# Kernel tuning notes

Measured on AMD Instinct MI355X. Metric: run time of the kernel, lower is better.

## Reference

```python
import jax, jax.numpy as jnp
import numpy as np


def setup_inputs() -> dict:
    key = jax.random.key(0)
    x = jax.random.normal(key, (8, 16, 256, 256, 3, 3), dtype=jnp.float32)
    return {"x": x, "padding_dim": 1}


def reference(x, padding_dim):
    """Vectorized SPD identity-pad: borders get eye(3), interior copies x.

    x: [B, C, H, W, 3, 3] -> [B, C, H+2p, W+2p, 3, 3]
    Faithful to the original quadruple-nested-loop `padding` function.
    """
    p = padding_dim
    B, C, H, W = x.shape[:4]
    # zero-pad spatial dims, then overwrite border cells with identity
    xp = jnp.pad(x, ((0, 0), (0, 0), (p, p), (p, p), (0, 0), (0, 0)))
    row = jnp.arange(H + 2 * p)
    col = jnp.arange(W + 2 * p)
    # border condition matches: i < p or (H+2p - i) <= p  (i.e. i >= H+p)
    row_border = (row < p) | (row >= H + p)          # [H+2p]
    col_border = (col < p) | (col >= W + p)          # [W+2p]
    border = row_border[:, None] | col_border[None, :]  # [H+2p, W+2p]
    eye = jnp.eye(3, dtype=x.dtype)
    out = jnp.where(border[None, None, :, :, None, None], eye, xp)
    return out
```

## Files before the change

kernel.cpp:

```cpp
#include <hip/hip_runtime.h>


constexpr int B  = 8;
constexpr int C  = 16;
constexpr int H  = 256;
constexpr int W  = 256;
constexpr int HP = 258;
constexpr int WP = 258;

constexpr int       IMGS    = B * C;
constexpr long long ROW_IN  = (long long)W * 9;
constexpr long long IMG_IN  = (long long)H * ROW_IN;
constexpr long long ROW_OUT = (long long)WP * 9;
constexpr long long IMG_OUT = (long long)HP * ROW_OUT;

constexpr int COPY_BLOCKS   = IMGS * H;
constexpr int BORDER_BLOCKS = 2048;
constexpr int       CELLS_PER_IMG = 2 * WP + 2 * H;
constexpr long long BORDER_FLOATS = (long long)IMGS * CELLS_PER_IMG * 9;

__global__ __launch_bounds__(192) void spd_pad_kernel(const float* __restrict__ x,
                                                      float* __restrict__ out) {
    const int blk = blockIdx.x;
    const int tid = threadIdx.x;

    if (blk < COPY_BLOCKS) {
        const int img = blk >> 8;
        const int i   = blk & 255;
        const float4* __restrict__ src =
            reinterpret_cast<const float4*>(x + (long long)img * IMG_IN + (long long)i * ROW_IN);
        float4* __restrict__ dst =
            reinterpret_cast<float4*>(out + (long long)img * IMG_OUT + (long long)(i + 1) * ROW_OUT + 9);
#pragma unroll
        for (int k = 0; k < 3; ++k) {
            const int idx = tid + k * 192;
            dst[idx] = src[idx];
        }
    } else {
        const long long stride = (long long)BORDER_BLOCKS * 192;
        long long t = (long long)(blk - COPY_BLOCKS) * 192 + tid;
        for (; t < BORDER_FLOATS; t += stride) {
            const int       e    = (int)(t % 9);
            const long long cell = t / 9;
            const int       k    = (int)(cell % CELLS_PER_IMG);
            const int       img  = (int)(cell / CELLS_PER_IMG);
            int i, j;
            if (k < WP) {
                i = 0;       j = k;
            } else if (k < 2 * WP) {
                i = HP - 1;  j = k - WP;
            } else if (k < 2 * WP + H) {
                j = 0;       i = k - 2 * WP + 1;
            } else {
                j = WP - 1;  i = k - (2 * WP + H) + 1;
            }
            const float v = (e == 0 || e == 4 || e == 8) ? 1.0f : 0.0f;
            out[(long long)img * IMG_OUT + (long long)i * ROW_OUT + (long long)j * 9 + e] = v;
        }
    }
}

extern "C" void kernel_launch(void* const* d_in, const int* in_sizes, int n_in,
                              void* d_out, int out_size, void* d_ws, size_t ws_size,
                              hipStream_t stream) {
    const float* x   = (const float*)d_in[0];
    float*       out = (float*)d_out;
    spd_pad_kernel<<<dim3(COPY_BLOCKS + BORDER_BLOCKS), dim3(192), 0, stream>>>(x, out);
}
```

Measured before the change: 493.9 us.

## Assign one block per output row and fuse border writes into row copies

The kernel now uses a 2D grid with one block per padded output row. Each interior row block copies its row and also writes the left and right identity cells itself. The top and bottom border rows are filled with vectorized float4 identity stores. This removes the separate grid-stride border pass, which used 64-bit divides and modulos and wrote scattered, uncoalesced floats. The cost is some extra per-block branching and small masked scalar stores at the row edges.

```diff
diff --git a/kernel.cpp b/kernel.cpp
--- a/kernel.cpp
+++ b/kernel.cpp
@@ -14,48 +14,44 @@
 constexpr long long ROW_OUT = (long long)WP * 9;
 constexpr long long IMG_OUT = (long long)HP * ROW_OUT;
 
-constexpr int COPY_BLOCKS   = IMGS * H;
-constexpr int BORDER_BLOCKS = 2048;
-constexpr int       CELLS_PER_IMG = 2 * WP + 2 * H;
-constexpr long long BORDER_FLOATS = (long long)IMGS * CELLS_PER_IMG * 9;
+constexpr int F4_PER_ROW_OUT = 580;
+constexpr int F4_PER_COPY    = 576;
 
 __global__ __launch_bounds__(192) void spd_pad_kernel(const float* __restrict__ x,
                                                       float* __restrict__ out) {
-    const int blk = blockIdx.x;
+    const int i   = blockIdx.x;
+    const int img = blockIdx.y;
     const int tid = threadIdx.x;
 
-    if (blk < COPY_BLOCKS) {
-        const int img = blk >> 8;
-        const int i   = blk & 255;
-        const float4* __restrict__ src =
-            reinterpret_cast<const float4*>(x + (long long)img * IMG_IN + (long long)i * ROW_IN);
-        float4* __restrict__ dst =
-            reinterpret_cast<float4*>(out + (long long)img * IMG_OUT + (long long)(i + 1) * ROW_OUT + 9);
+    float* __restrict__ rowp = out + (long long)img * IMG_OUT + (long long)i * ROW_OUT;
+
+    if (i != 0 && i != HP - 1) {
+        const float4* __restrict__ src4 =
+            reinterpret_cast<const float4*>(x + (long long)img * IMG_IN + (long long)(i - 1) * ROW_IN);
+        float4* __restrict__ dst4 = reinterpret_cast<float4*>(rowp + 9);
 #pragma unroll
         for (int k = 0; k < 3; ++k) {
             const int idx = tid + k * 192;
-            dst[idx] = src[idx];
+            dst4[idx] = src4[idx];
+        }
+        if (tid < 18) {
+            const int   e = (tid < 9) ? tid : tid - 9;
+            const float v = (e == 0 || e == 4 || e == 8) ? 1.0f : 0.0f;
+            rowp[(tid < 9) ? e : (2313 + e)] = v;
         }
     } else {
-        const long long stride = (long long)BORDER_BLOCKS * 192;
-        long long t = (long long)(blk - COPY_BLOCKS) * 192 + tid;
-        for (; t < BORDER_FLOATS; t += stride) {
-            const int       e    = (int)(t % 9);
-            const long long cell = t / 9;
-            const int       k    = (int)(cell % CELLS_PER_IMG);
-            const int       img  = (int)(cell / CELLS_PER_IMG);
-            int i, j;
-            if (k < WP) {
-                i = 0;       j = k;
-            } else if (k < 2 * WP) {
-                i = HP - 1;  j = k - WP;
-            } else if (k < 2 * WP + H) {
-                j = 0;       i = k - 2 * WP + 1;
-            } else {
-                j = WP - 1;  i = k - (2 * WP + H) + 1;
-            }
-            const float v = (e == 0 || e == 4 || e == 8) ? 1.0f : 0.0f;
-            out[(long long)img * IMG_OUT + (long long)i * ROW_OUT + (long long)j * 9 + e] = v;
+        float4* __restrict__ dst4 = reinterpret_cast<float4*>(rowp);
+        for (int f4 = tid; f4 < F4_PER_ROW_OUT; f4 += 192) {
+            int m = (f4 * 4) % 9;
+            float4 v;
+            v.x = (m == 0 || m == 4 || m == 8) ? 1.0f : 0.0f; m = (m == 8) ? 0 : m + 1;
+            v.y = (m == 0 || m == 4 || m == 8) ? 1.0f : 0.0f; m = (m == 8) ? 0 : m + 1;
+            v.z = (m == 0 || m == 4 || m == 8) ? 1.0f : 0.0f; m = (m == 8) ? 0 : m + 1;
+            v.w = (m == 0 || m == 4 || m == 8) ? 1.0f : 0.0f;
+            dst4[f4] = v;
+        }
+        if (tid < 2) {
+            rowp[2320 + tid] = (tid == 1) ? 1.0f : 0.0f;
         }
     }
 }
@@ -65,5 +61,5 @@
                               hipStream_t stream) {
     const float* x   = (const float*)d_in[0];
     float*       out = (float*)d_out;
-    spd_pad_kernel<<<dim3(COPY_BLOCKS + BORDER_BLOCKS), dim3(192), 0, stream>>>(x, out);
+    spd_pad_kernel<<<dim3(HP, IMGS), dim3(192), 0, stream>>>(x, out);
 }
```

Measured after the change: 488.5 us. About the same (-1.1%).
